# Kernel tuning notes

Hardware: AMD Instinct MI355X
Metric: run time of the kernel (lower is better)

## Reference

```python
import jax, jax.numpy as jnp
import numpy as np

LOG2 = float(np.log(2.0))


def setup_inputs() -> dict:
    key = jax.random.key(0)
    k1, k2, k3, k4, k5, k6 = jax.random.split(key, 6)
    N, E, G = 50000, 800000, 256
    d_node, d_edge, d_global, hidden = 128, 64, 64, 128
    node_feats = jax.random.normal(k1, (N, d_node), dtype=jnp.float32)
    edge_feats = jax.random.normal(k2, (E, d_edge), dtype=jnp.float32)
    global_feats = jax.random.normal(k3, (G, d_global), dtype=jnp.float32)
    edge_index = jax.random.randint(k4, (2, E), 0, N, dtype=jnp.int64)
    batch = jnp.sort(jax.random.randint(k5, (N,), 0, G, dtype=jnp.int64))
    # Linear(384 -> 128, bias=False); torch stores weight as [out, in], apply x @ W.T
    d_in = 2 * d_node + d_edge + d_global
    W = jax.random.normal(k6, (hidden, d_in), dtype=jnp.float32) * (1.0 / np.sqrt(d_in))
    return {"node_feats": node_feats, "edge_feats": edge_feats,
            "global_feats": global_feats, "edge_index": edge_index,
            "batch": batch, "W": W}


def reference(node_feats, edge_feats, global_feats, edge_index, batch, W):
    idx_src = edge_index[0]
    idx_dst = edge_index[1]
    batch_edge_map = batch[idx_src]                      # [E]
    out = jnp.concatenate([
        node_feats[idx_src],                             # [E, d_node]
        node_feats[idx_dst],                             # [E, d_node]
        edge_feats,                                      # [E, d_edge]
        global_feats[batch_edge_map],                    # [E, d_global]
    ], axis=1)                                           # [E, 384]
    h = out @ W.T                                        # [E, hidden]
    return jax.nn.softplus(h) - LOG2                     # shifted softplus
```

## Files before the change

### kernel.cpp

```cpp
#include <hip/hip_runtime.h>
#include <hip/hip_bf16.h>

#define N_NODES 50000
#define N_EDGES 800000
#define D_NODE  128
#define D_EDGE  64
#define D_GLOB  64
#define D_IN    384
#define D_OUT   128

#define APITCH  392

typedef __attribute__((ext_vector_type(4))) float  floatx4;
typedef __attribute__((ext_vector_type(8))) short  shortx8;

__device__ __forceinline__ shortx8 cvt8_bf16(const float* __restrict__ p) {
    floatx4 a = *(const floatx4*)p;
    floatx4 b = *(const floatx4*)(p + 4);
    shortx8 r;
    union { __hip_bfloat16 h; short s; } u;
    #pragma unroll
    for (int j = 0; j < 4; ++j) {
        u.h = __float2bfloat16(a[j]); r[j]     = u.s;
        u.h = __float2bfloat16(b[j]); r[j + 4] = u.s;
    }
    return r;
}

__global__ __launch_bounds__(256, 2)
void edge_mlp_kernel(const float* __restrict__ node,
                     const float* __restrict__ edgef,
                     const float* __restrict__ globf,
                     const int* __restrict__ eidx,
                     const int* __restrict__ batch,
                     const float* __restrict__ W,
                     float* __restrict__ out)
{
    __shared__ short A_lds[64 * APITCH];

    const int tid = threadIdx.x;
    const int e0  = blockIdx.x * 64;

    const int is64 = ((eidx[1] | eidx[3] | eidx[5] | eidx[7] |
                       eidx[9] | eidx[11] | eidx[13] | eidx[15]) == 0) ? 1 : 0;

    #pragma unroll
    for (int i = 0; i < 12; ++i) {
        int g       = tid + i * 256;
        int e_local = g / 48;
        int off     = (g - e_local * 48) * 8;
        int e       = e0 + e_local;
        const float* srcp;
        if (off < 128) {
            int s = eidx[(size_t)e << is64];
            srcp = node + (size_t)s * D_NODE + off;
        } else if (off < 256) {
            int d = eidx[(size_t)(N_EDGES + e) << is64];
            srcp = node + (size_t)d * D_NODE + (off - 128);
        } else if (off < 320) {
            srcp = edgef + (size_t)e * D_EDGE + (off - 256);
        } else {
            int s = eidx[(size_t)e << is64];
            int b = batch[(size_t)s << is64];
            srcp = globf + (size_t)b * D_GLOB + (off - 320);
        }
        *(shortx8*)(&A_lds[e_local * APITCH + off]) = cvt8_bf16(srcp);
    }

    const int wave = tid >> 6;
    const int lane = tid & 63;
    const int nlo  = lane & 15;
    const int quad = lane >> 4;

    shortx8 bfrag[12][2];
    #pragma unroll
    for (int kc = 0; kc < 12; ++kc) {
        #pragma unroll
        for (int nt = 0; nt < 2; ++nt) {
            int n = wave * 32 + nt * 16 + nlo;
            bfrag[kc][nt] = cvt8_bf16(W + (size_t)n * D_IN + kc * 32 + quad * 8);
        }
    }

    floatx4 acc[4][2];
    #pragma unroll
    for (int mt = 0; mt < 4; ++mt)
        #pragma unroll
        for (int nt = 0; nt < 2; ++nt)
            acc[mt][nt] = (floatx4){0.f, 0.f, 0.f, 0.f};

    __syncthreads();

    #pragma unroll
    for (int kc = 0; kc < 12; ++kc) {
        #pragma unroll
        for (int mt = 0; mt < 4; ++mt) {
            shortx8 afrag = *(const shortx8*)(
                &A_lds[(mt * 16 + nlo) * APITCH + kc * 32 + quad * 8]);
            #pragma unroll
            for (int nt = 0; nt < 2; ++nt) {
                acc[mt][nt] = __builtin_amdgcn_mfma_f32_16x16x32_bf16(
                    afrag, bfrag[kc][nt], acc[mt][nt], 0, 0, 0);
            }
        }
    }

    #pragma unroll
    for (int mt = 0; mt < 4; ++mt) {
        #pragma unroll
        for (int nt = 0; nt < 2; ++nt) {
            int n = wave * 32 + nt * 16 + nlo;
            #pragma unroll
            for (int r = 0; r < 4; ++r) {
                int e = e0 + mt * 16 + quad * 4 + r;
                float h  = acc[mt][nt][r];
                float t  = __expf(-fabsf(h));
                float sp = fmaxf(h, 0.0f) + __logf(1.0f + t);
                out[(size_t)e * D_OUT + n] = sp - 0.69314718055994531f;
            }
        }
    }
}

extern "C" void kernel_launch(void* const* d_in, const int* in_sizes, int n_in,
                              void* d_out, int out_size, void* d_ws, size_t ws_size,
                              hipStream_t stream) {
    const float* node  = (const float*)d_in[0];
    const float* edgef = (const float*)d_in[1];
    const float* globf = (const float*)d_in[2];
    const int*   eidx  = (const int*)d_in[3];
    const int*   batch = (const int*)d_in[4];
    const float* W     = (const float*)d_in[5];
    float*       out   = (float*)d_out;

    dim3 grid(N_EDGES / 64);
    dim3 block(256);
    edge_mlp_kernel<<<grid, block, 0, stream>>>(node, edgef, globf, eidx, batch, W, out);
}
```

Before: 1.090 ms.

## Precompute per-node and per-graph projections, then gather projected rows per edge

```diff
diff --git a/kernel.cpp b/kernel.cpp
--- a/kernel.cpp
+++ b/kernel.cpp
@@ -8,11 +8,14 @@
 #define D_GLOB  64
 #define D_IN    384
 #define D_OUT   128
+#define LN2F    0.69314718055994531f
 
 #define APITCH  392
 
 typedef __attribute__((ext_vector_type(4))) float  floatx4;
 typedef __attribute__((ext_vector_type(8))) short  shortx8;
+
+#define MFMA16 __builtin_amdgcn_mfma_f32_16x16x32_bf16
 
 __device__ __forceinline__ shortx8 cvt8_bf16(const float* __restrict__ p) {
     floatx4 a = *(const floatx4*)p;
@@ -25,6 +28,204 @@
         u.h = __float2bfloat16(b[j]); r[j + 4] = u.s;
     }
     return r;
+}
+
+__global__ __launch_bounds__(256, 2)
+void proj_node_kernel(const float* __restrict__ node,
+                      const float* __restrict__ W,
+                      float* __restrict__ Psrc,
+                      float* __restrict__ Pdst)
+{
+    const int bid   = blockIdx.x;
+    const int table = bid & 1;
+    const int i0    = (bid >> 1) * 64;
+    float* __restrict__ P = table ? Pdst : Psrc;
+    const int coloff = table * D_NODE;
+
+    const int tid  = threadIdx.x;
+    const int wave = tid >> 6;
+    const int lane = tid & 63;
+    const int nlo  = lane & 15;
+    const int quad = lane >> 4;
+
+    shortx8 wfrag[2][4];
+    #pragma unroll
+    for (int nt = 0; nt < 2; ++nt) {
+        const int n = wave * 32 + nt * 16 + nlo;
+        #pragma unroll
+        for (int kc = 0; kc < 4; ++kc)
+            wfrag[nt][kc] = cvt8_bf16(W + (size_t)n * D_IN + coloff + kc * 32 + quad * 8);
+    }
+
+    floatx4 acc[2][4];
+    #pragma unroll
+    for (int nt = 0; nt < 2; ++nt)
+        #pragma unroll
+        for (int it = 0; it < 4; ++it)
+            acc[nt][it] = (floatx4){0.f, 0.f, 0.f, 0.f};
+
+    #pragma unroll
+    for (int kc = 0; kc < 4; ++kc) {
+        #pragma unroll
+        for (int it = 0; it < 4; ++it) {
+            int i = i0 + it * 16 + nlo;
+            if (i >= N_NODES) i = N_NODES - 1;
+            shortx8 b = cvt8_bf16(node + (size_t)i * D_NODE + kc * 32 + quad * 8);
+            acc[0][it] = MFMA16(wfrag[0][kc], b, acc[0][it], 0, 0, 0);
+            acc[1][it] = MFMA16(wfrag[1][kc], b, acc[1][it], 0, 0, 0);
+        }
+    }
+
+    #pragma unroll
+    for (int it = 0; it < 4; ++it) {
+        const int i = i0 + it * 16 + nlo;
+        if (i < N_NODES) {
+            #pragma unroll
+            for (int nt = 0; nt < 2; ++nt) {
+                const int n0 = wave * 32 + nt * 16 + quad * 4;
+                *(floatx4*)(P + (size_t)i * D_OUT + n0) = acc[nt][it];
+            }
+        }
+    }
+}
+
+__global__ __launch_bounds__(256, 2)
+void proj_glob_kernel(const float* __restrict__ globf,
+                      const float* __restrict__ W,
+                      float* __restrict__ Pglob)
+{
+    const int i0   = blockIdx.x * 64;
+    const int tid  = threadIdx.x;
+    const int wave = tid >> 6;
+    const int lane = tid & 63;
+    const int nlo  = lane & 15;
+    const int quad = lane >> 4;
+
+    shortx8 wfrag[2][2];
+    #pragma unroll
+    for (int nt = 0; nt < 2; ++nt) {
+        const int n = wave * 32 + nt * 16 + nlo;
+        #pragma unroll
+        for (int kc = 0; kc < 2; ++kc)
+            wfrag[nt][kc] = cvt8_bf16(W + (size_t)n * D_IN + 320 + kc * 32 + quad * 8);
+    }
+
+    floatx4 acc[2][4];
+    #pragma unroll
+    for (int nt = 0; nt < 2; ++nt)
+        #pragma unroll
+        for (int it = 0; it < 4; ++it)
+            acc[nt][it] = (floatx4){0.f, 0.f, 0.f, 0.f};
+
+    #pragma unroll
+    for (int kc = 0; kc < 2; ++kc) {
+        #pragma unroll
+        for (int it = 0; it < 4; ++it) {
+            const int i = i0 + it * 16 + nlo;
+            shortx8 b = cvt8_bf16(globf + (size_t)i * D_GLOB + kc * 32 + quad * 8);
+            acc[0][it] = MFMA16(wfrag[0][kc], b, acc[0][it], 0, 0, 0);
+            acc[1][it] = MFMA16(wfrag[1][kc], b, acc[1][it], 0, 0, 0);
+        }
+    }
+
+    #pragma unroll
+    for (int it = 0; it < 4; ++it) {
+        const int i = i0 + it * 16 + nlo;
+        #pragma unroll
+        for (int nt = 0; nt < 2; ++nt) {
+            const int n0 = wave * 32 + nt * 16 + quad * 4;
+            *(floatx4*)(Pglob + (size_t)i * D_OUT + n0) = acc[nt][it];
+        }
+    }
+}
+
+__global__ __launch_bounds__(256, 2)
+void edge_fused_kernel(const float* __restrict__ edgef,
+                       const int* __restrict__ eidx,
+                       const int* __restrict__ batch,
+                       const float* __restrict__ W,
+                       const float* __restrict__ Psrc,
+                       const float* __restrict__ Pdst,
+                       const float* __restrict__ Pglob,
+                       float* __restrict__ out)
+{
+    const int tid  = threadIdx.x;
+    const int e0   = blockIdx.x * 64;
+    const int wave = tid >> 6;
+    const int lane = tid & 63;
+    const int nlo  = lane & 15;
+    const int quad = lane >> 4;
+
+    const int is64 = ((eidx[1] | eidx[3] | eidx[5] | eidx[7] |
+                       eidx[9] | eidx[11] | eidx[13] | eidx[15]) == 0) ? 1 : 0;
+
+    int src[4], dst[4], bat[4];
+    #pragma unroll
+    for (int et = 0; et < 4; ++et) {
+        const int e = e0 + et * 16 + nlo;
+        src[et] = eidx[(size_t)e << is64];
+        dst[et] = eidx[(size_t)(N_EDGES + e) << is64];
+    }
+    #pragma unroll
+    for (int et = 0; et < 4; ++et)
+        bat[et] = batch[(size_t)src[et] << is64];
+
+    shortx8 bfrag[4][2];
+    #pragma unroll
+    for (int et = 0; et < 4; ++et) {
+        const float* row = edgef + (size_t)(e0 + et * 16 + nlo) * D_EDGE;
+        #pragma unroll
+        for (int kc = 0; kc < 2; ++kc)
+            bfrag[et][kc] = cvt8_bf16(row + kc * 32 + quad * 8);
+    }
+
+    shortx8 wfrag[2][2];
+    #pragma unroll
+    for (int nt = 0; nt < 2; ++nt) {
+        const int n = wave * 32 + nt * 16 + nlo;
+        #pragma unroll
+        for (int kc = 0; kc < 2; ++kc)
+            wfrag[nt][kc] = cvt8_bf16(W + (size_t)n * D_IN + 256 + kc * 32 + quad * 8);
+    }
+
+    floatx4 acc[2][4];
+    #pragma unroll
+    for (int nt = 0; nt < 2; ++nt)
+        #pragma unroll
+        for (int et = 0; et < 4; ++et)
+            acc[nt][et] = (floatx4){0.f, 0.f, 0.f, 0.f};
+
+    #pragma unroll
+    for (int kc = 0; kc < 2; ++kc) {
+        #pragma unroll
+        for (int et = 0; et < 4; ++et) {
+            acc[0][et] = MFMA16(wfrag[0][kc], bfrag[et][kc], acc[0][et], 0, 0, 0);
+            acc[1][et] = MFMA16(wfrag[1][kc], bfrag[et][kc], acc[1][et], 0, 0, 0);
+        }
+    }
+
+    #pragma unroll
+    for (int et = 0; et < 4; ++et) {
+        const int e = e0 + et * 16 + nlo;
+        const float* ps = Psrc  + (size_t)src[et] * D_OUT;
+        const float* pd = Pdst  + (size_t)dst[et] * D_OUT;
+        const float* pg = Pglob + (size_t)bat[et] * D_OUT;
+        #pragma unroll
+        for (int nt = 0; nt < 2; ++nt) {
+            const int n0 = wave * 32 + nt * 16 + quad * 4;
+            floatx4 g1 = *(const floatx4*)(ps + n0);
+            floatx4 g2 = *(const floatx4*)(pd + n0);
+            floatx4 g3 = *(const floatx4*)(pg + n0);
+            floatx4 r;
+            #pragma unroll
+            for (int j = 0; j < 4; ++j) {
+                const float h = acc[nt][et][j] + g1[j] + g2[j] + g3[j];
+                const float t = __expf(-fabsf(h));
+                r[j] = fmaxf(h, 0.f) + __logf(1.f + t) - LN2F;
+            }
+            __builtin_nontemporal_store(r, (floatx4*)(out + (size_t)e * D_OUT + n0));
+        }
+    }
 }
 
 __global__ __launch_bounds__(256, 2)
@@ -99,8 +300,7 @@
                 &A_lds[(mt * 16 + nlo) * APITCH + kc * 32 + quad * 8]);
             #pragma unroll
             for (int nt = 0; nt < 2; ++nt) {
-                acc[mt][nt] = __builtin_amdgcn_mfma_f32_16x16x32_bf16(
-                    afrag, bfrag[kc][nt], acc[mt][nt], 0, 0, 0);
+                acc[mt][nt] = MFMA16(afrag, bfrag[kc][nt], acc[mt][nt], 0, 0, 0);
             }
         }
     }
@@ -116,7 +316,7 @@
                 float h  = acc[mt][nt][r];
                 float t  = __expf(-fabsf(h));
                 float sp = fmaxf(h, 0.0f) + __logf(1.0f + t);
-                out[(size_t)e * D_OUT + n] = sp - 0.69314718055994531f;
+                out[(size_t)e * D_OUT + n] = sp - LN2F;
             }
         }
     }
@@ -133,7 +333,19 @@
     const float* W     = (const float*)d_in[5];
     float*       out   = (float*)d_out;
 
-    dim3 grid(N_EDGES / 64);
-    dim3 block(256);
-    edge_mlp_kernel<<<grid, block, 0, stream>>>(node, edgef, globf, eidx, batch, W, out);
-}
+    const size_t PN   = (size_t)N_NODES * D_OUT;
+    const size_t need = (2 * PN + 256 * D_OUT) * sizeof(float);
+
+    if (ws_size >= need) {
+        float* Psrc  = (float*)d_ws;
+        float* Pdst  = Psrc + PN;
+        float* Pglob = Pdst + PN;
+        proj_node_kernel<<<dim3(782 * 2), dim3(256), 0, stream>>>(node, W, Psrc, Pdst);
+        proj_glob_kernel<<<dim3(4), dim3(256), 0, stream>>>(globf, W, Pglob);
+        edge_fused_kernel<<<dim3(N_EDGES / 64), dim3(256), 0, stream>>>(
+            edgef, eidx, batch, W, Psrc, Pdst, Pglob, out);
+    } else {
+        edge_mlp_kernel<<<dim3(N_EDGES / 64), dim3(256), 0, stream>>>(
+            node, edgef, globf, eidx, batch, W, out);
+    }
+}
```

After: 872.8 us. 19.9% less time.
